# Kernel tuning notes

Hardware: AMD Instinct MI355X
Metric: run time of the kernel (lower is better)

Reference implementation:

```python
import jax, jax.numpy as jnp
import numpy as np

LENGTHSCALE = 1.0


def setup_inputs() -> dict:
    key = jax.random.key(0)
    k1, k2, k3 = jax.random.split(key, 3)
    M, N, D = 4096, 8192, 256
    X = jax.random.normal(k1, (M, D), dtype=jnp.float32)
    X_train = jax.random.normal(k2, (N, D), dtype=jnp.float32)
    alpha = jax.random.normal(k3, (N, 1), dtype=jnp.float32)
    return {"X": X, "X_train": X_train, "alpha": alpha}


def _rbf_kernel(X1, X2, lengthscale=LENGTHSCALE):
    # Same math as sum((X1[:,None]-X2[None,:])**2, -1) without the [M,N,D] tensor.
    sq1 = jnp.sum(X1 * X1, axis=-1, keepdims=True)          # [M,1]
    sq2 = jnp.sum(X2 * X2, axis=-1)                         # [N]
    dist_sq = sq1 + sq2[None, :] - 2.0 * (X1 @ X2.T)        # [M,N]
    return jnp.exp(-dist_sq / (2.0 * lengthscale ** 2))


def reference(X, X_train, alpha):
    K_star = _rbf_kernel(X, X_train)    # [M,N]
    pred = K_star @ alpha               # [M,1]
    return pred
```

## Files before the change

### kernel.cpp

```cpp
#include <hip/hip_runtime.h>
#include <hip/hip_bf16.h>

#define M_DIM 4096
#define N_DIM 8192
#define D_DIM 256
#define NSLICE 32
#define NCHUNK 16
#define C_EXP (-0.7213475204444817f)
#define K_ACC (1.4426950408889634f)
#define SKIP_THR (-151.0f)
#define WLDS 18432

typedef __attribute__((ext_vector_type(8))) short short8;
typedef __attribute__((ext_vector_type(4))) float f32x4;

__device__ inline unsigned short f2bf(float f) {
    __hip_bfloat16 h = __float2bfloat16(f);
    return *reinterpret_cast<unsigned short*>(&h);
}

__global__ __launch_bounds__(256) void prep_kernel(
    const float* __restrict__ X, const float* __restrict__ T,
    const float* __restrict__ alpha,
    unsigned short* __restrict__ Xb, unsigned short* __restrict__ Tb,
    float* __restrict__ sq1, float2* __restrict__ sqal)
{
    const int row  = blockIdx.x * 4 + (threadIdx.x >> 6);
    const int lane = threadIdx.x & 63;
    const float* src; unsigned short* dst; int r; bool isX;
    if (row < M_DIM) { src = X; dst = Xb; r = row; isX = true; }
    else             { src = T; dst = Tb; r = row - M_DIM; isX = false; }

    const float4* s4 = reinterpret_cast<const float4*>(src + (size_t)r * D_DIM);
    float4 v = s4[lane];
    float ss = v.x * v.x + v.y * v.y + v.z * v.z + v.w * v.w;

    ushort4 b4;
    b4.x = f2bf(v.x); b4.y = f2bf(v.y); b4.z = f2bf(v.z); b4.w = f2bf(v.w);
    reinterpret_cast<ushort4*>(dst + (size_t)r * D_DIM)[lane] = b4;

    #pragma unroll
    for (int o = 1; o < 64; o <<= 1) ss += __shfl_xor(ss, o);
    if (lane == 0) {
        if (isX) sq1[r] = ss * C_EXP;
        else     sqal[r] = make_float2(ss * C_EXP, alpha[r]);
    }
}

__global__ __launch_bounds__(256, 2) void gemm_kernel(
    const unsigned short* __restrict__ Xb, const unsigned short* __restrict__ Tb,
    const float* __restrict__ sq1, const float2* __restrict__ sqal,
    float* __restrict__ part)
{
    __shared__ __align__(16) char smem[4 * WLDS];
    const int cslice = blockIdx.x & 31;
    const int quad   = blockIdx.x >> 5;
    const int wid    = threadIdx.x >> 6;
    const int lane   = threadIdx.x & 63;
    const int l15    = lane & 15;
    const int lg     = lane >> 4;

    char* wlds = smem + wid * WLDS;
    const int rowbase = quad * 256 + wid * 64;
    const int colbase = cslice * 256;

    short8 af[4][8];
    #pragma unroll
    for (int m = 0; m < 4; ++m)
        #pragma unroll
        for (int ks = 0; ks < 8; ++ks)
            af[m][ks] = *(const short8*)(Xb +
                (size_t)(rowbase + m * 16 + l15) * D_DIM + ks * 32 + lg * 8);

    float4 s1v[4];
    #pragma unroll
    for (int m = 0; m < 4; ++m)
        s1v[m] = *reinterpret_cast<const float4*>(sq1 + rowbase + m * 16 + lg * 4);
    float s1max = -1e30f;
    #pragma unroll
    for (int m = 0; m < 4; ++m)
        #pragma unroll
        for (int r = 0; r < 4; ++r) s1max = fmaxf(s1max, s1v[m][r]);

    asm volatile("s_waitcnt vmcnt(0)" ::: "memory");

    const char* TbB = (const char*)Tb;
    const char* SaB = (const char*)sqal;

    auto stage = [&](int i) {
        const int b = i & 1;
        char* bufB = wlds + b * 8192;
        #pragma unroll
        for (int j = 0; j < 8; ++j) {
            const int col_local = j * 2 + (lane >> 5);
            const size_t src = (size_t)(colbase + i * 16 + col_local) * 512
                             + (size_t)(((lane & 31) ^ (col_local & 7)) * 16);
            __builtin_amdgcn_global_load_lds(
                (const __attribute__((address_space(1))) void*)(TbB + src),
                (__attribute__((address_space(3))) void*)(bufB + j * 1024), 16, 0, 0);
        }
        const size_t ssrc = (size_t)(colbase + i * 16) * 8 + (lane & 7) * 16;
        __builtin_amdgcn_global_load_lds(
            (const __attribute__((address_space(1))) void*)(SaB + ssrc),
            (__attribute__((address_space(3))) void*)(wlds + 16384 + b * 1024), 16, 0, 0);
    };

    float psum[4][4];
    #pragma unroll
    for (int m = 0; m < 4; ++m)
        #pragma unroll
        for (int r = 0; r < 4; ++r) psum[m][r] = 0.0f;

    auto compute = [&](int i) {
        const int b = i & 1;
        const char* bufB = wlds + b * 8192;
        f32x4 acc[4];
        #pragma unroll
        for (int m = 0; m < 4; ++m) acc[m] = (f32x4)0.0f;
        #pragma unroll
        for (int ks = 0; ks < 8; ++ks) {
            const short8 bf = *(const short8*)(bufB + l15 * 512 +
                (((ks * 4 + lg) ^ (l15 & 7)) * 16));
            #pragma unroll
            for (int m = 0; m < 4; ++m)
                acc[m] = __builtin_amdgcn_mfma_f32_16x16x32_bf16(
                    af[m][ks], bf, acc[m], 0, 0, 0);
        }
        const float2 sa = *(const float2*)(wlds + 16384 + b * 1024 + l15 * 8);
        float amax = acc[0][0];
        #pragma unroll
        for (int m = 0; m < 4; ++m)
            #pragma unroll
            for (int r = 0; r < 4; ++r) amax = fmaxf(amax, acc[m][r]);
        const float bound = fmaf(amax, K_ACC, s1max + sa.x);
        if (!__all(bound < SKIP_THR)) {
            #pragma unroll
            for (int m = 0; m < 4; ++m)
                #pragma unroll
                for (int r = 0; r < 4; ++r) {
                    const float arg = fmaf(acc[m][r], K_ACC, s1v[m][r] + sa.x);
                    psum[m][r] = fmaf(__builtin_amdgcn_exp2f(arg), sa.y, psum[m][r]);
                }
        }
    };

    stage(0);
    #pragma unroll 1
    for (int i = 0; i < NCHUNK - 1; ++i) {
        stage(i + 1);
        asm volatile("s_waitcnt vmcnt(9)" ::: "memory");
        compute(i);
    }
    asm volatile("s_waitcnt vmcnt(0)" ::: "memory");
    compute(NCHUNK - 1);

    #pragma unroll
    for (int m = 0; m < 4; ++m) {
        float4 pv;
        #pragma unroll
        for (int r = 0; r < 4; ++r) {
            float p = psum[m][r];
            p += __shfl_xor(p, 1);
            p += __shfl_xor(p, 2);
            p += __shfl_xor(p, 4);
            p += __shfl_xor(p, 8);
            ((float*)&pv)[r] = p;
        }
        if (l15 == 0)
            *reinterpret_cast<float4*>(part + (size_t)cslice * M_DIM +
                                       rowbase + m * 16 + lg * 4) = pv;
    }
}

__global__ __launch_bounds__(256) void reduce_kernel(
    const float* __restrict__ part, float* __restrict__ out)
{
    const int gi = blockIdx.x * 256 + threadIdx.x;
    float s = 0.0f;
    #pragma unroll
    for (int b = 0; b < NSLICE; ++b) s += part[(size_t)b * M_DIM + gi];
    out[gi] = s;
}

extern "C" void kernel_launch(void* const* d_in, const int* in_sizes, int n_in,
                              void* d_out, int out_size, void* d_ws, size_t ws_size,
                              hipStream_t stream)
{
    const float* X  = (const float*)d_in[0];
    const float* T  = (const float*)d_in[1];
    const float* al = (const float*)d_in[2];
    float* out = (float*)d_out;

    char* ws = (char*)d_ws;
    unsigned short* Xb = (unsigned short*)ws;
    unsigned short* Tb = (unsigned short*)(ws + (size_t)M_DIM * D_DIM * 2);
    float* sq1  = (float*)(ws + (size_t)(M_DIM + N_DIM) * D_DIM * 2);
    float2* sqal = (float2*)(sq1 + M_DIM);
    float* part = (float*)(sqal + N_DIM);

    prep_kernel<<<(M_DIM + N_DIM) / 4, 256, 0, stream>>>(X, T, al, Xb, Tb, sq1, sqal);
    gemm_kernel<<<16 * NSLICE, 256, 0, stream>>>(Xb, Tb, sq1, sqal, part);
    reduce_kernel<<<M_DIM / 256, 256, 0, stream>>>(part, out);
}
```

Before: 37.44 us.

## Share B-tile LDS staging across waves with quad-buffered cooperative loads

Each wave used to stage the full 16-column training tile into its own private LDS region, so all four waves in a block loaded identical data. Now the four waves each load a quarter of the tile into one shared quad-buffered LDS ring, guarded by a block barrier. Prefetch depth goes from one chunk ahead to two. The squared-norm/alpha vector for the whole column slice is loaded once up front instead of per chunk, and the main loop is fully unrolled. Global-to-LDS traffic per block drops fourfold and LDS use shrinks, at the cost of one barrier per chunk.

```diff
diff --git a/kernel.cpp b/kernel.cpp
--- a/kernel.cpp
+++ b/kernel.cpp
@@ -9,7 +9,9 @@
 #define C_EXP (-0.7213475204444817f)
 #define K_ACC (1.4426950408889634f)
 #define SKIP_THR (-151.0f)
-#define WLDS 18432
+#define BUFB 8192
+#define SQAL_OFF (4 * BUFB)
+#define LDS_BYTES (4 * BUFB + 2048)
 
 typedef __attribute__((ext_vector_type(8))) short short8;
 typedef __attribute__((ext_vector_type(4))) float f32x4;
@@ -52,7 +54,7 @@
     const float* __restrict__ sq1, const float2* __restrict__ sqal,
     float* __restrict__ part)
 {
-    __shared__ __align__(16) char smem[4 * WLDS];
+    __shared__ __align__(16) char smem[LDS_BYTES];
     const int cslice = blockIdx.x & 31;
     const int quad   = blockIdx.x >> 5;
     const int wid    = threadIdx.x >> 6;
@@ -60,7 +62,6 @@
     const int l15    = lane & 15;
     const int lg     = lane >> 4;
 
-    char* wlds = smem + wid * WLDS;
     const int rowbase = quad * 256 + wid * 64;
     const int colbase = cslice * 256;
 
@@ -85,24 +86,26 @@
     asm volatile("s_waitcnt vmcnt(0)" ::: "memory");
 
     const char* TbB = (const char*)Tb;
-    const char* SaB = (const char*)sqal;
+    const char* SaB = (const char*)sqal + (size_t)colbase * 8;
+
+    #pragma unroll
+    for (int s = 0; s < 2; ++s)
+        __builtin_amdgcn_global_load_lds(
+            (const __attribute__((address_space(1))) void*)(SaB + s * 1024 + lane * 16),
+            (__attribute__((address_space(3))) void*)(smem + SQAL_OFF + s * 1024), 16, 0, 0);
 
     auto stage = [&](int i) {
-        const int b = i & 1;
-        char* bufB = wlds + b * 8192;
-        #pragma unroll
-        for (int j = 0; j < 8; ++j) {
+        char* buf = smem + (i & 3) * BUFB;
+        #pragma unroll
+        for (int c = 0; c < 2; ++c) {
+            const int j = wid * 2 + c;
             const int col_local = j * 2 + (lane >> 5);
             const size_t src = (size_t)(colbase + i * 16 + col_local) * 512
-                             + (size_t)(((lane & 31) ^ (col_local & 7)) * 16);
+                             + (size_t)((((lane & 31) ^ (col_local & 7)) * 16));
             __builtin_amdgcn_global_load_lds(
                 (const __attribute__((address_space(1))) void*)(TbB + src),
-                (__attribute__((address_space(3))) void*)(bufB + j * 1024), 16, 0, 0);
-        }
-        const size_t ssrc = (size_t)(colbase + i * 16) * 8 + (lane & 7) * 16;
-        __builtin_amdgcn_global_load_lds(
-            (const __attribute__((address_space(1))) void*)(SaB + ssrc),
-            (__attribute__((address_space(3))) void*)(wlds + 16384 + b * 1024), 16, 0, 0);
+                (__attribute__((address_space(3))) void*)(buf + j * 1024), 16, 0, 0);
+        }
     };
 
     float psum[4][4];
@@ -112,21 +115,20 @@
         for (int r = 0; r < 4; ++r) psum[m][r] = 0.0f;
 
     auto compute = [&](int i) {
-        const int b = i & 1;
-        const char* bufB = wlds + b * 8192;
+        const char* buf = smem + (i & 3) * BUFB;
         f32x4 acc[4];
         #pragma unroll
         for (int m = 0; m < 4; ++m) acc[m] = (f32x4)0.0f;
         #pragma unroll
         for (int ks = 0; ks < 8; ++ks) {
-            const short8 bf = *(const short8*)(bufB + l15 * 512 +
+            const short8 bf = *(const short8*)(buf + l15 * 512 +
                 (((ks * 4 + lg) ^ (l15 & 7)) * 16));
             #pragma unroll
             for (int m = 0; m < 4; ++m)
                 acc[m] = __builtin_amdgcn_mfma_f32_16x16x32_bf16(
                     af[m][ks], bf, acc[m], 0, 0, 0);
         }
-        const float2 sa = *(const float2*)(wlds + 16384 + b * 1024 + l15 * 8);
+        const float2 sa = *(const float2*)(smem + SQAL_OFF + (i * 16 + l15) * 8);
         float amax = acc[0][0];
         #pragma unroll
         for (int m = 0; m < 4; ++m)
@@ -145,14 +147,20 @@
     };
 
     stage(0);
-    #pragma unroll 1
-    for (int i = 0; i < NCHUNK - 1; ++i) {
-        stage(i + 1);
-        asm volatile("s_waitcnt vmcnt(9)" ::: "memory");
+    stage(1);
+    #pragma unroll
+    for (int i = 0; i < NCHUNK; ++i) {
+        if (i + 2 < NCHUNK) {
+            stage(i + 2);
+            asm volatile("s_waitcnt vmcnt(4)" ::: "memory");
+        } else if (i + 1 < NCHUNK) {
+            asm volatile("s_waitcnt vmcnt(2)" ::: "memory");
+        } else {
+            asm volatile("s_waitcnt vmcnt(0)" ::: "memory");
+        }
+        __builtin_amdgcn_s_barrier();
         compute(i);
     }
-    asm volatile("s_waitcnt vmcnt(0)" ::: "memory");
-    compute(NCHUNK - 1);
 
     #pragma unroll
     for (int m = 0; m < 4; ++m) {
```

Result: faster. 34.45 us (-8.0%).
